# Performance work log

Hardware: AMD Instinct MI355X
Metric: run time of the kernel (lower is better)

Reference implementation:

```python
import jax, jax.numpy as jnp
import numpy as np

B, S, N, E = 8, 32, 2000, 64000
GH, H = 32, 64  # gat_h, lstm hidden
NEG_SLOPE = 0.2


def setup_inputs() -> dict:
    key = jax.random.key(0)
    ks = jax.random.split(key, 12)
    f32 = jnp.float32
    x = jax.random.normal(ks[0], (B, S, N), f32)
    edge_index = jax.random.randint(ks[1], (2, E), 0, N)
    # GATConv(1, GH, heads=1, concat=False): lin weight [GH,1] -> vector, att_src/att_dst [GH], bias [GH]
    w_lin = jax.random.normal(ks[2], (GH,), f32)
    att_src = jax.random.normal(ks[3], (GH,), f32) * 0.1
    att_dst = jax.random.normal(ks[4], (GH,), f32) * 0.1
    gat_bias = jax.random.normal(ks[5], (GH,), f32) * 0.01
    D = GH * N  # LSTM input size
    W_ih = jax.random.normal(ks[6], (4 * H, D), f32) * (1.0 / np.sqrt(D))
    W_hh = jax.random.normal(ks[7], (4 * H, H), f32) * (1.0 / np.sqrt(H))
    b_ih = jax.random.normal(ks[8], (4 * H,), f32) * 0.01
    b_hh = jax.random.normal(ks[9], (4 * H,), f32) * 0.01
    W_head = jax.random.normal(ks[10], (N, H), f32) * (1.0 / np.sqrt(H))
    b_head = jax.random.normal(ks[11], (N,), f32) * 0.01
    return {"x": x, "edge_index": edge_index, "w_lin": w_lin, "att_src": att_src,
            "att_dst": att_dst, "gat_bias": gat_bias, "W_ih": W_ih, "W_hh": W_hh,
            "b_ih": b_ih, "b_hh": b_hh, "W_head": W_head, "b_head": b_head}


def reference(x, edge_index, w_lin, att_src, att_dst, gat_bias,
              W_ih, W_hh, b_ih, b_hh, W_head, b_head):
    x = x.astype(jnp.float32)
    # --- GAT (in_channels=1, heads=1), batched over (B,S) ---
    # PyG default: add self-loops
    loops = jnp.arange(N)
    ei = jnp.concatenate([edge_index, jnp.stack([loops, loops])], axis=1)
    src, dst = ei[0], ei[1]  # [Et], Et = E + N
    # lifted feature h_n = x_n * w_lin (rank-1), so attention logits are scalar per node
    a_src = x * jnp.dot(w_lin, att_src)  # [B,S,N]
    a_dst = x * jnp.dot(w_lin, att_dst)  # [B,S,N]
    e = jax.nn.leaky_relu(a_src[..., src] + a_dst[..., dst], NEG_SLOPE)  # [B,S,Et]
    e = jnp.moveaxis(e, -1, 0)  # [Et,B,S] (segment axis leading)
    seg_max = jax.ops.segment_max(e, dst, num_segments=N)  # [N,B,S]
    e = jnp.exp(e - seg_max[dst])
    denom = jax.ops.segment_sum(e, dst, num_segments=N)  # [N,B,S]
    alpha = e / denom[dst]  # edge softmax over incoming edges
    x_src = jnp.moveaxis(x[..., src], -1, 0)  # [Et,B,S]
    agg = jax.ops.segment_sum(alpha * x_src, dst, num_segments=N)  # [N,B,S]
    agg = jnp.moveaxis(agg, 0, -1)  # [B,S,N]
    # outer product with w_lin restores [.,GH]; add bias, then relu (from forward)
    h = jax.nn.relu(agg[..., None] * w_lin + gat_bias)  # [B,S,N,GH]
    lstm_in = h.reshape(B, S, N * GH)

    # --- LSTM (1 layer, batch_first), keep final hidden state ---
    def step(carry, xt):
        hp, cp = carry
        gates = xt @ W_ih.T + b_ih + hp @ W_hh.T + b_hh  # [B,4H]
        i, f, g, o = jnp.split(gates, 4, axis=-1)
        c = jax.nn.sigmoid(f) * cp + jax.nn.sigmoid(i) * jnp.tanh(g)
        hn = jax.nn.sigmoid(o) * jnp.tanh(c)
        return (hn, c), None

    h0 = jnp.zeros((B, H), jnp.float32)
    c0 = jnp.zeros((B, H), jnp.float32)
    (hT, _), _ = jax.lax.scan(step, (h0, c0), jnp.swapaxes(lstm_in, 0, 1))
    return hT @ W_head.T + b_head  # [B,N]
```

## Files before the change

### kernel.cpp

```cpp
#include <hip/hip_runtime.h>
#include <hip/hip_bf16.h>
#include <cstddef>
#include <cstdint>

#define B_  8
#define S_  32
#define BT_ 256
#define N_  2000
#define E_  64000
#define GH_ 32
#define H_  64
#define G4_ 256
#define D_  64000
#define NEG_SLOPE_ 0.2f

#define KC_   125
#define NPC_  16

typedef __attribute__((ext_vector_type(8))) short short8;
typedef __attribute__((ext_vector_type(4))) float floatx4;
union U8 { uint32_t u[4]; short8 s; };

__device__ __forceinline__ float fsigmoid(float x) { return 1.0f / (1.0f + __expf(-x)); }
__device__ __forceinline__ float ftanh_(float x)   { return 1.0f - 2.0f / (__expf(2.0f * x) + 1.0f); }

__device__ __forceinline__ void split2(float v0, float v1, uint32_t& hi, uint32_t& lo) {
  uint32_t b0 = __float_as_uint(v0), b1 = __float_as_uint(v1);
  hi = __builtin_amdgcn_perm(b1, b0, 0x07060302u);
  float l0 = v0 - __uint_as_float(b0 & 0xffff0000u);
  float l1 = v1 - __uint_as_float(b1 & 0xffff0000u);
  lo = __builtin_amdgcn_perm(__float_as_uint(l1), __float_as_uint(l0), 0x07060302u);
}


__global__ __launch_bounds__(256) void hist_kernel(
    const int* __restrict__ ei, int* __restrict__ deg)
{
  const int i = blockIdx.x * 256 + threadIdx.x;
  if (i < E_) atomicAdd(&deg[ei[E_ + i]], 1);
}

__global__ __launch_bounds__(256) void scan_kernel(
    const int* __restrict__ deg, int* __restrict__ rowptr, int* __restrict__ cursor)
{
  __shared__ int tsum[256];
  const int tid = threadIdx.x;
  int v[8];
  int s = 0;
  const int base = tid * 8;
#pragma unroll
  for (int j = 0; j < 8; ++j) {
    const int idx = base + j;
    const int d = (idx < N_) ? deg[idx] : 0;
    v[j] = s;
    s += d;
  }
  tsum[tid] = s;
  __syncthreads();
  for (int off = 1; off < 256; off <<= 1) {
    int t = 0;
    if (tid >= off) t = tsum[tid - off];
    __syncthreads();
    tsum[tid] += t;
    __syncthreads();
  }
  const int ebase = tsum[tid] - s;
#pragma unroll
  for (int j = 0; j < 8; ++j) {
    const int idx = base + j;
    if (idx < N_) {
      const int r = ebase + v[j];
      rowptr[idx] = r;
      cursor[idx] = r;
    }
  }
  if (tid == 0) rowptr[N_] = E_;
}

__global__ __launch_bounds__(256) void scatter_kernel(
    const int* __restrict__ ei, int* __restrict__ cursor, int* __restrict__ csr_src)
{
  const int i = blockIdx.x * 256 + threadIdx.x;
  if (i >= E_) return;
  const int s = ei[i];
  const int d = ei[E_ + i];
  const int pos = atomicAdd(&cursor[d], 1);
  csr_src[pos] = s;
}

__global__ __launch_bounds__(256) void transpose_kernel(
    const float* __restrict__ x, float* __restrict__ xT)
{
  __shared__ float tile[32][33];
  const int tx = threadIdx.x & 31;
  const int ty = threadIdx.x >> 5;
  const int n0  = blockIdx.x * 32;
  const int bt0 = blockIdx.y * 32;
#pragma unroll
  for (int r = 0; r < 4; ++r) {
    const int bt = bt0 + ty + r * 8;
    const int nn = n0 + tx;
    if (nn < N_) tile[ty + r * 8][tx] = x[(size_t)bt * N_ + nn];
  }
  __syncthreads();
#pragma unroll
  for (int r = 0; r < 4; ++r) {
    const int n = n0 + ty + r * 8;
    if (n < N_) xT[(size_t)n * BT_ + bt0 + tx] = tile[tx][ty + r * 8];
  }
}

__global__ __launch_bounds__(256) void gat_gather_kernel(
    const float* __restrict__ xT, const int* __restrict__ rowptr,
    const int* __restrict__ csr_src,
    const float* __restrict__ w_lin, const float* __restrict__ att_src,
    const float* __restrict__ att_dst, float* __restrict__ agg_T)
{
  __shared__ int srcs[512];
  const int n   = blockIdx.x;
  const int tid = threadIdx.x;

  float c_s = 0.f, c_d = 0.f;
  for (int g = 0; g < GH_; ++g) {
    const float w = w_lin[g];
    c_s += w * att_src[g];
    c_d += w * att_dst[g];
  }

  const int r0 = rowptr[n];
  const int r1 = rowptr[n + 1];
  const int d  = r1 - r0;
  for (int i = tid; i < d && i < 512; i += 256) srcs[i] = csr_src[r0 + i];
  __syncthreads();

  const float xn = xT[(size_t)n * BT_ + tid];
  float e = (c_s + c_d) * xn;
  e = e > 0.f ? e : NEG_SLOPE_ * e;
  float w = __expf(e);
  float num = w * xn;
  float den = w;

  for (int p = 0; p < d; ++p) {
    int s;
    if (p < 512) s = srcs[p]; else s = csr_src[r0 + p];
    const float xs = xT[(size_t)s * BT_ + tid];
    float ee = c_s * xs + c_d * xn;
    ee = ee > 0.f ? ee : NEG_SLOPE_ * ee;
    const float ww = __expf(ee);
    num += ww * xs;
    den += ww;
  }
  agg_T[(size_t)n * BT_ + tid] = num / den;
}

__global__ __launch_bounds__(256) void gate_mfma_kernel(
    const float* __restrict__ W_ih, const float* __restrict__ agg_T,
    const float* __restrict__ w_lin, const float* __restrict__ gat_bias,
    float* __restrict__ partial, float* __restrict__ pre_gates, int use_atomic)
{
  __shared__ float agg_s[NPC_ * 256];

  const int tid  = threadIdx.x;
  const int nb   = blockIdx.x;
  const int kc   = blockIdx.y;
  const int n0   = kc * NPC_;
  const int wv   = tid >> 6;
  const int lane = tid & 63;
  const int i16  = lane & 15;
  const int q    = lane >> 4;
  const int j0   = nb * 64;

  {
    const float4* src = (const float4*)(agg_T + (size_t)n0 * 256);
    float4* dst = (float4*)agg_s;
#pragma unroll
    for (int p = 0; p < 4; ++p) dst[tid + p * 256] = src[tid + p * 256];
  }

  float wlr[8], gbr[8];
#pragma unroll
  for (int jx = 0; jx < 8; ++jx) {
    wlr[jx] = w_lin[q * 8 + jx];
    gbr[jx] = gat_bias[q * 8 + jx];
  }

  floatx4 acc[4][4];
#pragma unroll
  for (int mt = 0; mt < 4; ++mt)
#pragma unroll
    for (int jt = 0; jt < 4; ++jt)
#pragma unroll
      for (int r = 0; r < 4; ++r) acc[mt][jt][r] = 0.f;

  __syncthreads();

  const float* Wr0 = W_ih + (size_t)(j0 +  0 + i16) * D_ + (size_t)n0 * GH_ + q * 8;
  const float* Wr1 = W_ih + (size_t)(j0 + 16 + i16) * D_ + (size_t)n0 * GH_ + q * 8;
  const float* Wr2 = W_ih + (size_t)(j0 + 32 + i16) * D_ + (size_t)n0 * GH_ + q * 8;
  const float* Wr3 = W_ih + (size_t)(j0 + 48 + i16) * D_ + (size_t)n0 * GH_ + q * 8;

#pragma unroll 1
  for (int nn = 0; nn < NPC_; ++nn) {
    float4 b0[4], b1[4];
    b0[0] = *(const float4*)(Wr0 + nn * GH_);     b1[0] = *(const float4*)(Wr0 + nn * GH_ + 4);
    b0[1] = *(const float4*)(Wr1 + nn * GH_);     b1[1] = *(const float4*)(Wr1 + nn * GH_ + 4);
    b0[2] = *(const float4*)(Wr2 + nn * GH_);     b1[2] = *(const float4*)(Wr2 + nn * GH_ + 4);
    b0[3] = *(const float4*)(Wr3 + nn * GH_);     b1[3] = *(const float4*)(Wr3 + nn * GH_ + 4);

    short8 ah[4], al[4];
#pragma unroll
    for (int mt = 0; mt < 4; ++mt) {
      const float a = agg_s[nn * 256 + wv * 64 + mt * 16 + i16];
      U8 Hh, Ll;
#pragma unroll
      for (int p = 0; p < 4; ++p) {
        float v0 = fmaf(a, wlr[2 * p],     gbr[2 * p]);
        float v1 = fmaf(a, wlr[2 * p + 1], gbr[2 * p + 1]);
        v0 = fmaxf(v0, 0.f);
        v1 = fmaxf(v1, 0.f);
        split2(v0, v1, Hh.u[p], Ll.u[p]);
      }
      ah[mt] = Hh.s; al[mt] = Ll.s;
    }

#pragma unroll
    for (int jt = 0; jt < 4; ++jt) {
      short8 bh, bl;
      {
        U8 Hh, Ll;
        split2(b0[jt].x, b0[jt].y, Hh.u[0], Ll.u[0]);
        split2(b0[jt].z, b0[jt].w, Hh.u[1], Ll.u[1]);
        split2(b1[jt].x, b1[jt].y, Hh.u[2], Ll.u[2]);
        split2(b1[jt].z, b1[jt].w, Hh.u[3], Ll.u[3]);
        bh = Hh.s; bl = Ll.s;
      }
#pragma unroll
      for (int mt = 0; mt < 4; ++mt) {
        acc[mt][jt] = __builtin_amdgcn_mfma_f32_16x16x32_bf16(ah[mt], bh, acc[mt][jt], 0, 0, 0);
        acc[mt][jt] = __builtin_amdgcn_mfma_f32_16x16x32_bf16(al[mt], bh, acc[mt][jt], 0, 0, 0);
        acc[mt][jt] = __builtin_amdgcn_mfma_f32_16x16x32_bf16(ah[mt], bl, acc[mt][jt], 0, 0, 0);
      }
    }
  }

#pragma unroll
  for (int mt = 0; mt < 4; ++mt) {
    const int bt = wv * 64 + mt * 16 + q * 4;
#pragma unroll
    for (int jt = 0; jt < 4; ++jt) {
      const int j = j0 + jt * 16 + i16;
      if (use_atomic) {
#pragma unroll
        for (int r = 0; r < 4; ++r) atomicAdd(&pre_gates[(bt + r) * G4_ + j], acc[mt][jt][r]);
      } else {
#pragma unroll
        for (int r = 0; r < 4; ++r)
          partial[((size_t)kc * 256 + (bt + r)) * 256 + j] = acc[mt][jt][r];
      }
    }
  }
}

__global__ __launch_bounds__(256) void reduce_kernel(
    const float* __restrict__ partial, float* __restrict__ pre_gates)
{
  const int o = blockIdx.x * 256 + threadIdx.x;
  float s0 = 0.f, s1 = 0.f, s2 = 0.f, s3 = 0.f;
  int kc = 0;
  for (; kc + 4 <= KC_; kc += 4) {
    s0 += partial[(size_t)(kc + 0) * 65536 + o];
    s1 += partial[(size_t)(kc + 1) * 65536 + o];
    s2 += partial[(size_t)(kc + 2) * 65536 + o];
    s3 += partial[(size_t)(kc + 3) * 65536 + o];
  }
  for (; kc < KC_; ++kc) s0 += partial[(size_t)kc * 65536 + o];
  pre_gates[o] = (s0 + s1) + (s2 + s3);
}

__global__ __launch_bounds__(256) void lstm_kernel(
    const float* __restrict__ pre_gates, const float* __restrict__ W_hh,
    const float* __restrict__ b_ih, const float* __restrict__ b_hh,
    float* __restrict__ hT)
{
  const int b   = blockIdx.x;
  const int tid = threadIdx.x;
  __shared__ float h_s[H_];
  __shared__ float g_s[G4_];

  float wr[H_];
#pragma unroll
  for (int k = 0; k < H_; ++k) wr[k] = W_hh[(size_t)tid * H_ + k];

  float pg[S_];
#pragma unroll
  for (int t = 0; t < S_; ++t) pg[t] = pre_gates[(size_t)(b * S_ + t) * G4_ + tid];

  const float bias = b_ih[tid] + b_hh[tid];
  if (tid < H_) h_s[tid] = 0.f;
  float c = 0.f;
  __syncthreads();

  for (int t = 0; t < S_; ++t) {
    float g0 = pg[t] + bias, g1 = 0.f, g2 = 0.f, g3 = 0.f;
#pragma unroll
    for (int k = 0; k < H_; k += 4) {
      g0 = fmaf(wr[k + 0], h_s[k + 0], g0);
      g1 = fmaf(wr[k + 1], h_s[k + 1], g1);
      g2 = fmaf(wr[k + 2], h_s[k + 2], g2);
      g3 = fmaf(wr[k + 3], h_s[k + 3], g3);
    }
    g_s[tid] = (g0 + g1) + (g2 + g3);
    __syncthreads();
    if (tid < H_) {
      const float ig = fsigmoid(g_s[tid]);
      const float fg = fsigmoid(g_s[H_ + tid]);
      const float gg = ftanh_(g_s[2 * H_ + tid]);
      const float og = fsigmoid(g_s[3 * H_ + tid]);
      c = fg * c + ig * gg;
      h_s[tid] = og * ftanh_(c);
    }
    __syncthreads();
  }
  if (tid < H_) hT[b * H_ + tid] = h_s[tid];
}

__global__ __launch_bounds__(256) void head_kernel(
    const float* __restrict__ hT, const float* __restrict__ W_head,
    const float* __restrict__ b_head, float* __restrict__ out)
{
  const int o = blockIdx.x * 256 + threadIdx.x;
  if (o >= B_ * N_) return;
  const int b = o / N_;
  const int n = o - b * N_;
  const float4* w4 = (const float4*)(W_head + (size_t)n * H_);
  const float4* h4 = (const float4*)(hT + (size_t)b * H_);
  float acc = b_head[n];
#pragma unroll
  for (int q = 0; q < H_ / 4; ++q) {
    const float4 w = w4[q];
    const float4 h = h4[q];
    acc += w.x * h.x + w.y * h.y + w.z * h.z + w.w * h.w;
  }
  out[o] = acc;
}

extern "C" void kernel_launch(void* const* d_in, const int* in_sizes, int n_in,
                              void* d_out, int out_size, void* d_ws, size_t ws_size,
                              hipStream_t stream) {
  const float* x        = (const float*)d_in[0];
  const int*   ei       = (const int*)  d_in[1];
  const float* w_lin    = (const float*)d_in[2];
  const float* att_src  = (const float*)d_in[3];
  const float* att_dst  = (const float*)d_in[4];
  const float* gat_bias = (const float*)d_in[5];
  const float* W_ih     = (const float*)d_in[6];
  const float* W_hh     = (const float*)d_in[7];
  const float* b_ih     = (const float*)d_in[8];
  const float* b_hh     = (const float*)d_in[9];
  const float* W_head   = (const float*)d_in[10];
  const float* b_head   = (const float*)d_in[11];
  float* out = (float*)d_out;

  char* ws = (char*)d_ws;
  float* agg_T     = (float*)(ws + 0);
  float* pre_gates = (float*)(ws + 2048000);
  float* hT        = (float*)(ws + 2310144);
  float* xT        = (float*)(ws + 2312192);
  int*   deg       = (int*)  (ws + 4360192);
  int*   rowptr    = (int*)  (ws + 4368384);
  int*   cursor    = (int*)  (ws + 4376576);
  int*   csr_src   = (int*)  (ws + 4384768);
  float* partial   = (float*)(ws + 4640768);
  const size_t need = 4640768 + (size_t)KC_ * 65536 * sizeof(float);
  const int use_atomic = (ws_size < need) ? 1 : 0;

  hipMemsetAsync(deg, 0, N_ * sizeof(int), stream);
  hist_kernel<<<dim3((E_ + 255) / 256), dim3(256), 0, stream>>>(ei, deg);
  scan_kernel<<<dim3(1), dim3(256), 0, stream>>>(deg, rowptr, cursor);
  scatter_kernel<<<dim3((E_ + 255) / 256), dim3(256), 0, stream>>>(ei, cursor, csr_src);
  transpose_kernel<<<dim3((N_ + 31) / 32, BT_ / 32), dim3(256), 0, stream>>>(x, xT);
  gat_gather_kernel<<<dim3(N_), dim3(256), 0, stream>>>(
      xT, rowptr, csr_src, w_lin, att_src, att_dst, agg_T);

  if (use_atomic) {
    hipMemsetAsync(pre_gates, 0, G4_ * BT_ * sizeof(float), stream);
  }
  gate_mfma_kernel<<<dim3(4, KC_), dim3(256), 0, stream>>>(
      W_ih, agg_T, w_lin, gat_bias, partial, pre_gates, use_atomic);
  if (!use_atomic) {
    reduce_kernel<<<dim3(256), dim3(256), 0, stream>>>(partial, pre_gates);
  }

  lstm_kernel<<<dim3(B_), dim3(256), 0, stream>>>(pre_gates, W_hh, b_ih, b_hh, hT);
  head_kernel<<<dim3((B_ * N_ + 255) / 256), dim3(256), 0, stream>>>(hT, W_head, b_head, out);
}
```

Before: 225.2 us.

## Split gate MFMA grid over batch-time halves and prefetch W_ih rows

The gate projection kernel gains a third grid dimension that splits the 256 batch-time rows into two halves of 128. This doubles the block count and halves per-block accumulators and shared memory, which should raise occupancy and latency hiding. The W_ih loads for the next node are also issued one iteration ahead in registers, so the global-load latency overlaps the MFMA work. The cost is that each W_ih tile is now read by two blocks, so DRAM traffic may double unless L2 or the last-level cache catches the second read. Register pressure also rises from the prefetch buffers.

```diff
diff --git a/kernel.cpp b/kernel.cpp
--- a/kernel.cpp
+++ b/kernel.cpp
@@ -158,11 +158,12 @@
     const float* __restrict__ w_lin, const float* __restrict__ gat_bias,
     float* __restrict__ partial, float* __restrict__ pre_gates, int use_atomic)
 {
-  __shared__ float agg_s[NPC_ * 256];
+  __shared__ float agg_s[NPC_ * 128];
 
   const int tid  = threadIdx.x;
   const int nb   = blockIdx.x;
   const int kc   = blockIdx.y;
+  const int z    = blockIdx.z;
   const int n0   = kc * NPC_;
   const int wv   = tid >> 6;
   const int lane = tid & 63;
@@ -171,10 +172,15 @@
   const int j0   = nb * 64;
 
   {
-    const float4* src = (const float4*)(agg_T + (size_t)n0 * 256);
+    const float4* src = (const float4*)agg_T;
     float4* dst = (float4*)agg_s;
 #pragma unroll
-    for (int p = 0; p < 4; ++p) dst[tid + p * 256] = src[tid + p * 256];
+    for (int p = 0; p < 2; ++p) {
+      const int f   = tid + p * 256;
+      const int row = f >> 5;
+      const int col = f & 31;
+      dst[f] = src[(size_t)(n0 + row) * 64 + z * 32 + col];
+    }
   }
 
   float wlr[8], gbr[8];
@@ -184,9 +190,9 @@
     gbr[jx] = gat_bias[q * 8 + jx];
   }
 
-  floatx4 acc[4][4];
-#pragma unroll
-  for (int mt = 0; mt < 4; ++mt)
+  floatx4 acc[2][4];
+#pragma unroll
+  for (int mt = 0; mt < 2; ++mt)
 #pragma unroll
     for (int jt = 0; jt < 4; ++jt)
 #pragma unroll
@@ -194,23 +200,29 @@
 
   __syncthreads();
 
-  const float* Wr0 = W_ih + (size_t)(j0 +  0 + i16) * D_ + (size_t)n0 * GH_ + q * 8;
-  const float* Wr1 = W_ih + (size_t)(j0 + 16 + i16) * D_ + (size_t)n0 * GH_ + q * 8;
-  const float* Wr2 = W_ih + (size_t)(j0 + 32 + i16) * D_ + (size_t)n0 * GH_ + q * 8;
-  const float* Wr3 = W_ih + (size_t)(j0 + 48 + i16) * D_ + (size_t)n0 * GH_ + q * 8;
+  const float* Wb = W_ih + (size_t)(j0 + i16) * D_ + (size_t)n0 * GH_ + q * 8;
+
+  float4 cb[8];
+#pragma unroll
+  for (int jt = 0; jt < 4; ++jt) {
+    cb[2 * jt]     = *(const float4*)(Wb + (size_t)jt * 16 * D_);
+    cb[2 * jt + 1] = *(const float4*)(Wb + (size_t)jt * 16 * D_ + 4);
+  }
 
 #pragma unroll 1
   for (int nn = 0; nn < NPC_; ++nn) {
-    float4 b0[4], b1[4];
-    b0[0] = *(const float4*)(Wr0 + nn * GH_);     b1[0] = *(const float4*)(Wr0 + nn * GH_ + 4);
-    b0[1] = *(const float4*)(Wr1 + nn * GH_);     b1[1] = *(const float4*)(Wr1 + nn * GH_ + 4);
-    b0[2] = *(const float4*)(Wr2 + nn * GH_);     b1[2] = *(const float4*)(Wr2 + nn * GH_ + 4);
-    b0[3] = *(const float4*)(Wr3 + nn * GH_);     b1[3] = *(const float4*)(Wr3 + nn * GH_ + 4);
-
-    short8 ah[4], al[4];
-#pragma unroll
-    for (int mt = 0; mt < 4; ++mt) {
-      const float a = agg_s[nn * 256 + wv * 64 + mt * 16 + i16];
+    const int nnx = (nn + 1) & (NPC_ - 1);
+    float4 pb[8];
+#pragma unroll
+    for (int jt = 0; jt < 4; ++jt) {
+      pb[2 * jt]     = *(const float4*)(Wb + (size_t)jt * 16 * D_ + nnx * GH_);
+      pb[2 * jt + 1] = *(const float4*)(Wb + (size_t)jt * 16 * D_ + nnx * GH_ + 4);
+    }
+
+    short8 ah[2], al[2];
+#pragma unroll
+    for (int mt = 0; mt < 2; ++mt) {
+      const float a = agg_s[nn * 128 + wv * 32 + mt * 16 + i16];
       U8 Hh, Ll;
 #pragma unroll
       for (int p = 0; p < 4; ++p) {
@@ -228,24 +240,27 @@
       short8 bh, bl;
       {
         U8 Hh, Ll;
-        split2(b0[jt].x, b0[jt].y, Hh.u[0], Ll.u[0]);
-        split2(b0[jt].z, b0[jt].w, Hh.u[1], Ll.u[1]);
-        split2(b1[jt].x, b1[jt].y, Hh.u[2], Ll.u[2]);
-        split2(b1[jt].z, b1[jt].w, Hh.u[3], Ll.u[3]);
+        split2(cb[2 * jt].x,     cb[2 * jt].y,     Hh.u[0], Ll.u[0]);
+        split2(cb[2 * jt].z,     cb[2 * jt].w,     Hh.u[1], Ll.u[1]);
+        split2(cb[2 * jt + 1].x, cb[2 * jt + 1].y, Hh.u[2], Ll.u[2]);
+        split2(cb[2 * jt + 1].z, cb[2 * jt + 1].w, Hh.u[3], Ll.u[3]);
         bh = Hh.s; bl = Ll.s;
       }
 #pragma unroll
-      for (int mt = 0; mt < 4; ++mt) {
+      for (int mt = 0; mt < 2; ++mt) {
         acc[mt][jt] = __builtin_amdgcn_mfma_f32_16x16x32_bf16(ah[mt], bh, acc[mt][jt], 0, 0, 0);
         acc[mt][jt] = __builtin_amdgcn_mfma_f32_16x16x32_bf16(al[mt], bh, acc[mt][jt], 0, 0, 0);
         acc[mt][jt] = __builtin_amdgcn_mfma_f32_16x16x32_bf16(ah[mt], bl, acc[mt][jt], 0, 0, 0);
       }
     }
-  }
-
-#pragma unroll
-  for (int mt = 0; mt < 4; ++mt) {
-    const int bt = wv * 64 + mt * 16 + q * 4;
+
+#pragma unroll
+    for (int u = 0; u < 8; ++u) cb[u] = pb[u];
+  }
+
+#pragma unroll
+  for (int mt = 0; mt < 2; ++mt) {
+    const int bt = z * 128 + wv * 32 + mt * 16 + q * 4;
 #pragma unroll
     for (int jt = 0; jt < 4; ++jt) {
       const int j = j0 + jt * 16 + i16;
@@ -385,7 +400,7 @@
   if (use_atomic) {
     hipMemsetAsync(pre_gates, 0, G4_ * BT_ * sizeof(float), stream);
   }
-  gate_mfma_kernel<<<dim3(4, KC_), dim3(256), 0, stream>>>(
+  gate_mfma_kernel<<<dim3(4, KC_, 2), dim3(256), 0, stream>>>(
       W_ih, agg_T, w_lin, gat_bias, partial, pre_gates, use_atomic);
   if (!use_atomic) {
     reduce_kernel<<<dim3(256), dim3(256), 0, stream>>>(partial, pre_gates);
```

Result: slower. 251.1 us (+11.5%).

## Unroll GAT gather, software-pipeline W_ih loads, split gate tiles for occupancy

Applied to the files above, without the earlier changes.

The GAT gather now stages source indices in 512-entry chunks and unrolls the edge loop by four, so several independent global loads are in flight at once. The gate MFMA kernel halves the output columns per block (32 instead of 64) and doubles the grid. It adds register double-buffering that prefetches the next node's W_ih slice, and sets launch bounds to request three waves per SIMD. The aim is more parallelism and hidden memory latency on the W_ih stream and the irregular gathers. The cost is that each block converts the agg tile (ah/al) for fewer output columns, so that conversion work is repeated across twice as many blocks.

```diff
diff --git a/kernel.cpp b/kernel.cpp
--- a/kernel.cpp
+++ b/kernel.cpp
@@ -121,6 +121,7 @@
   const int tid = threadIdx.x;
 
   float c_s = 0.f, c_d = 0.f;
+#pragma unroll
   for (int g = 0; g < GH_; ++g) {
     const float w = w_lin[g];
     c_s += w * att_src[g];
@@ -130,30 +131,52 @@
   const int r0 = rowptr[n];
   const int r1 = rowptr[n + 1];
   const int d  = r1 - r0;
-  for (int i = tid; i < d && i < 512; i += 256) srcs[i] = csr_src[r0 + i];
-  __syncthreads();
 
   const float xn = xT[(size_t)n * BT_ + tid];
+  const float ad = c_d * xn;
   float e = (c_s + c_d) * xn;
   e = e > 0.f ? e : NEG_SLOPE_ * e;
   float w = __expf(e);
   float num = w * xn;
   float den = w;
 
-  for (int p = 0; p < d; ++p) {
-    int s;
-    if (p < 512) s = srcs[p]; else s = csr_src[r0 + p];
-    const float xs = xT[(size_t)s * BT_ + tid];
-    float ee = c_s * xs + c_d * xn;
-    ee = ee > 0.f ? ee : NEG_SLOPE_ * ee;
-    const float ww = __expf(ee);
-    num += ww * xs;
-    den += ww;
+  for (int base = 0; base < d; base += 512) {
+    const int cnt = min(512, d - base);
+    __syncthreads();
+    for (int i = tid; i < cnt; i += 256) srcs[i] = csr_src[r0 + base + i];
+    __syncthreads();
+
+    int p = 0;
+    for (; p + 4 <= cnt; p += 4) {
+      const int s0 = srcs[p], s1 = srcs[p + 1], s2 = srcs[p + 2], s3 = srcs[p + 3];
+      const float x0 = xT[(size_t)s0 * BT_ + tid];
+      const float x1 = xT[(size_t)s1 * BT_ + tid];
+      const float x2 = xT[(size_t)s2 * BT_ + tid];
+      const float x3 = xT[(size_t)s3 * BT_ + tid];
+      float e0 = fmaf(c_s, x0, ad); e0 = e0 > 0.f ? e0 : NEG_SLOPE_ * e0;
+      float e1 = fmaf(c_s, x1, ad); e1 = e1 > 0.f ? e1 : NEG_SLOPE_ * e1;
+      float e2 = fmaf(c_s, x2, ad); e2 = e2 > 0.f ? e2 : NEG_SLOPE_ * e2;
+      float e3 = fmaf(c_s, x3, ad); e3 = e3 > 0.f ? e3 : NEG_SLOPE_ * e3;
+      const float w0 = __expf(e0), w1 = __expf(e1), w2 = __expf(e2), w3 = __expf(e3);
+      num = fmaf(w0, x0, num); den += w0;
+      num = fmaf(w1, x1, num); den += w1;
+      num = fmaf(w2, x2, num); den += w2;
+      num = fmaf(w3, x3, num); den += w3;
+    }
+    for (; p < cnt; ++p) {
+      const int s = srcs[p];
+      const float xs = xT[(size_t)s * BT_ + tid];
+      float ee = fmaf(c_s, xs, ad);
+      ee = ee > 0.f ? ee : NEG_SLOPE_ * ee;
+      const float ww = __expf(ee);
+      num = fmaf(ww, xs, num);
+      den += ww;
+    }
   }
   agg_T[(size_t)n * BT_ + tid] = num / den;
 }
 
-__global__ __launch_bounds__(256) void gate_mfma_kernel(
+__global__ __launch_bounds__(256, 3) void gate_mfma_kernel(
     const float* __restrict__ W_ih, const float* __restrict__ agg_T,
     const float* __restrict__ w_lin, const float* __restrict__ gat_bias,
     float* __restrict__ partial, float* __restrict__ pre_gates, int use_atomic)
@@ -168,7 +191,7 @@
   const int lane = tid & 63;
   const int i16  = lane & 15;
   const int q    = lane >> 4;
-  const int j0   = nb * 64;
+  const int j0   = nb * 32;
 
   {
     const float4* src = (const float4*)(agg_T + (size_t)n0 * 256);
@@ -184,28 +207,34 @@
     gbr[jx] = gat_bias[q * 8 + jx];
   }
 
-  floatx4 acc[4][4];
+  floatx4 acc[4][2];
 #pragma unroll
   for (int mt = 0; mt < 4; ++mt)
 #pragma unroll
-    for (int jt = 0; jt < 4; ++jt)
+    for (int jt = 0; jt < 2; ++jt)
 #pragma unroll
       for (int r = 0; r < 4; ++r) acc[mt][jt][r] = 0.f;
 
   __syncthreads();
 
-  const float* Wr0 = W_ih + (size_t)(j0 +  0 + i16) * D_ + (size_t)n0 * GH_ + q * 8;
-  const float* Wr1 = W_ih + (size_t)(j0 + 16 + i16) * D_ + (size_t)n0 * GH_ + q * 8;
-  const float* Wr2 = W_ih + (size_t)(j0 + 32 + i16) * D_ + (size_t)n0 * GH_ + q * 8;
-  const float* Wr3 = W_ih + (size_t)(j0 + 48 + i16) * D_ + (size_t)n0 * GH_ + q * 8;
+  const float* Wb = W_ih + (size_t)(j0 + i16) * D_ + (size_t)n0 * GH_ + q * 8;
+
+  float4 cb[4];
+#pragma unroll
+  for (int jt = 0; jt < 2; ++jt) {
+    cb[2 * jt]     = *(const float4*)(Wb + (size_t)jt * 16 * D_);
+    cb[2 * jt + 1] = *(const float4*)(Wb + (size_t)jt * 16 * D_ + 4);
+  }
 
 #pragma unroll 1
   for (int nn = 0; nn < NPC_; ++nn) {
-    float4 b0[4], b1[4];
-    b0[0] = *(const float4*)(Wr0 + nn * GH_);     b1[0] = *(const float4*)(Wr0 + nn * GH_ + 4);
-    b0[1] = *(const float4*)(Wr1 + nn * GH_);     b1[1] = *(const float4*)(Wr1 + nn * GH_ + 4);
-    b0[2] = *(const float4*)(Wr2 + nn * GH_);     b1[2] = *(const float4*)(Wr2 + nn * GH_ + 4);
-    b0[3] = *(const float4*)(Wr3 + nn * GH_);     b1[3] = *(const float4*)(Wr3 + nn * GH_ + 4);
+    const int nnx = (nn + 1) & (NPC_ - 1);
+    float4 pb[4];
+#pragma unroll
+    for (int jt = 0; jt < 2; ++jt) {
+      pb[2 * jt]     = *(const float4*)(Wb + (size_t)jt * 16 * D_ + nnx * GH_);
+      pb[2 * jt + 1] = *(const float4*)(Wb + (size_t)jt * 16 * D_ + nnx * GH_ + 4);
+    }
 
     short8 ah[4], al[4];
 #pragma unroll
@@ -224,14 +253,14 @@
     }
 
 #pragma unroll
-    for (int jt = 0; jt < 4; ++jt) {
+    for (int jt = 0; jt < 2; ++jt) {
       short8 bh, bl;
       {
         U8 Hh, Ll;
-        split2(b0[jt].x, b0[jt].y, Hh.u[0], Ll.u[0]);
-        split2(b0[jt].z, b0[jt].w, Hh.u[1], Ll.u[1]);
-        split2(b1[jt].x, b1[jt].y, Hh.u[2], Ll.u[2]);
-        split2(b1[jt].z, b1[jt].w, Hh.u[3], Ll.u[3]);
+        split2(cb[2 * jt].x,     cb[2 * jt].y,     Hh.u[0], Ll.u[0]);
+        split2(cb[2 * jt].z,     cb[2 * jt].w,     Hh.u[1], Ll.u[1]);
+        split2(cb[2 * jt + 1].x, cb[2 * jt + 1].y, Hh.u[2], Ll.u[2]);
+        split2(cb[2 * jt + 1].z, cb[2 * jt + 1].w, Hh.u[3], Ll.u[3]);
         bh = Hh.s; bl = Ll.s;
       }
 #pragma unroll
@@ -241,13 +270,16 @@
         acc[mt][jt] = __builtin_amdgcn_mfma_f32_16x16x32_bf16(ah[mt], bl, acc[mt][jt], 0, 0, 0);
       }
     }
+
+#pragma unroll
+    for (int u = 0; u < 4; ++u) cb[u] = pb[u];
   }
 
 #pragma unroll
   for (int mt = 0; mt < 4; ++mt) {
     const int bt = wv * 64 + mt * 16 + q * 4;
 #pragma unroll
-    for (int jt = 0; jt < 4; ++jt) {
+    for (int jt = 0; jt < 2; ++jt) {
       const int j = j0 + jt * 16 + i16;
       if (use_atomic) {
 #pragma unroll
@@ -385,7 +417,7 @@
   if (use_atomic) {
     hipMemsetAsync(pre_gates, 0, G4_ * BT_ * sizeof(float), stream);
   }
-  gate_mfma_kernel<<<dim3(4, KC_), dim3(256), 0, stream>>>(
+  gate_mfma_kernel<<<dim3(8, KC_), dim3(256), 0, stream>>>(
       W_ih, agg_T, w_lin, gat_bias, partial, pre_gates, use_atomic);
   if (!use_atomic) {
     reduce_kernel<<<dim3(256), dim3(256), 0, stream>>>(partial, pre_gates);
```

Result: slower. 240.2 us (+6.7%).
